# Kernel tuning notes

Measured on AMD Instinct MI355X. Metric: run time of the kernel, lower is better.

## Reference

```python
import jax, jax.numpy as jnp
import numpy as np

B, V_IN, V_OUT, F_IN, F_OUT, N_CP = 100000, 128, 128, 512, 512, 16
DIM_H = max(V_IN, V_OUT)  # hidden_vectors=None -> max(dim_vectors_in, dim_vectors_out)
EPS = 1e-8


def setup_inputs() -> dict:
    key = jax.random.key(0)
    ks = jax.random.split(key, 9)
    u = lambda k, shape, scale: jax.random.uniform(k, shape, jnp.float32, -scale, scale)
    wh_k = 1.0 / np.sqrt(V_IN).astype(np.float32)
    wu_k = 1.0 / np.sqrt(DIM_H + N_CP).astype(np.float32)
    f_in = DIM_H + N_CP + F_IN  # 656
    kf = 1.0 / np.sqrt(f_in).astype(np.float32)
    kg = 1.0 / np.sqrt(F_OUT).astype(np.float32)
    return {
        "feats": jax.random.normal(ks[0], (B, F_IN), jnp.float32),
        "vectors": jax.random.normal(ks[1], (B, V_IN, 3), jnp.float32),
        "Wh": u(ks[2], (V_IN, DIM_H), wh_k),
        "Wcp": u(ks[3], (V_IN, 2 * N_CP), wh_k),
        "Wu": u(ks[4], (DIM_H + N_CP, V_OUT), wu_k),
        "Wf": u(ks[5], (f_in, F_OUT), kf),      # torch Linear weight, stored (in,out)
        "bf": u(ks[6], (F_OUT,), kf),
        "Wg": u(ks[7], (F_OUT, V_OUT), kg),
        "bg": u(ks[8], (V_OUT,), kg),
    }


def reference(feats, vectors, Wh, Wcp, Wu, Wf, bf, Wg, bg):
    # vectors: [b, v_in, 3]; mix vector channels (matmul acts per xyz component c)
    Vh = jnp.einsum('bvc,vh->bhc', vectors, Wh)            # [b, dim_h, 3]
    # cross-product features
    Vcp = jnp.einsum('bvc,vp->bpc', vectors, Wcp)          # [b, 2*n_cp, 3]
    cp = jnp.cross(Vcp[:, :N_CP], Vcp[:, N_CP:])           # [b, n_cp, 3]
    Vh = jnp.concatenate([Vh, cp], axis=1)                 # [b, dim_h+n_cp, 3]
    Vu = jnp.einsum('bkc,ko->boc', Vh, Wu)                 # [b, v_out, 3]
    # clamped L2 norm over xyz
    sh = jnp.sqrt(jnp.maximum(jnp.sum(Vh * Vh, axis=-1), EPS))  # [b, dim_h+n_cp]
    s = jnp.concatenate([feats, sh], axis=1)               # [b, dim_h+n_cp+f_in]
    feats_out = jax.nn.silu(s @ Wf + bf)                   # [b, f_out]
    gating = feats_out @ Wg + bg                           # [b, v_out]
    vectors_out = jax.nn.sigmoid(gating)[..., None] * Vu   # [b, v_out, 3]
    return feats_out, vectors_out
```

## Files before the change

### kernel.cpp

```cpp
#include <hip/hip_runtime.h>

#define BATCH 100000
#define M3 300000
#define VECBASE 51200000
#define KP 704

typedef float fl4  __attribute__((ext_vector_type(4)));
typedef float f32x4 __attribute__((ext_vector_type(4)));
typedef short s16x4 __attribute__((ext_vector_type(4)));
typedef short s16x8 __attribute__((ext_vector_type(8)));

__device__ __forceinline__ short f2bf(float f) {
  unsigned int u = __float_as_uint(f);
  u += 0x7fffu + ((u >> 16) & 1u);
  return (short)(u >> 16);
}
__device__ __forceinline__ float bf2f(short s) {
  return __uint_as_float(((unsigned int)(unsigned short)s) << 16);
}
__device__ __forceinline__ s16x8 pack8(fl4 a, fl4 b) {
  s16x8 o;
  o[0] = f2bf(a[0]); o[1] = f2bf(a[1]); o[2] = f2bf(a[2]); o[3] = f2bf(a[3]);
  o[4] = f2bf(b[0]); o[5] = f2bf(b[1]); o[6] = f2bf(b[2]); o[7] = f2bf(b[3]);
  return o;
}
__device__ __forceinline__ void glds16(const void* g, void* l) {
  __builtin_amdgcn_global_load_lds((const __attribute__((address_space(1))) void*)g,
                                   (__attribute__((address_space(3))) void*)l, 16, 0, 0);
}
#define WAITBAR(N) asm volatile("s_waitcnt vmcnt(" #N ")\ns_barrier" ::: "memory")

__global__ __launch_bounds__(256) void prep_w(
    const float* __restrict__ feats, const float* __restrict__ Wh,
    const float* __restrict__ Wcp, const float* __restrict__ Wu,
    const float* __restrict__ Wf, const float* __restrict__ Wg,
    short* __restrict__ Ab, short* __restrict__ WB1, short* __restrict__ WuTp,
    short* __restrict__ WfT, short* __restrict__ WgT) {
  const int tid = blockIdx.x * 256 + threadIdx.x;
  const int stride = gridDim.x * 256;
  for (int i = tid; i < 6400000; i += stride) {
    int b = i >> 6, kk = (i & 63) * 8;
    fl4 v0 = *reinterpret_cast<const fl4*>(&feats[(size_t)b * 512 + kk]);
    fl4 v1 = *reinterpret_cast<const fl4*>(&feats[(size_t)b * 512 + kk + 4]);
    *(s16x8*)&Ab[(size_t)b * KP + kk] = pack8(v0, v1);
  }
  for (int gid = tid; gid < 466944; gid += stride) {
    if (gid < 20480) {
      int n = gid >> 7, k = gid & 127;
      WB1[gid] = f2bf(n < 128 ? Wh[k * 128 + n] : Wcp[k * 32 + (n - 128)]);
    } else if (gid < 40960) {
      int i = gid - 20480;
      int o = i / 160, k = i - o * 160;
      WuTp[i] = k < 144 ? f2bf(Wu[k * 128 + o]) : (short)0;
    } else if (gid < 401408) {
      int i = gid - 40960;
      int n = i / KP, k = i - n * KP;
      WfT[i] = k < 656 ? f2bf(Wf[k * 512 + n]) : (short)0;
    } else {
      int i = gid - 401408;
      int n = i >> 9, k = i & 511;
      WgT[i] = f2bf(Wg[k * 128 + n]);
    }
  }
}

__global__ __launch_bounds__(256) void geo_fused(
    const float* __restrict__ vecs, const short* __restrict__ WB1,
    const short* __restrict__ WuTp, short* __restrict__ Ab,
    short* __restrict__ Vub) {
  __shared__ __align__(16) short U[96 * 168];
  const int t = threadIdx.x;
  const int b0 = blockIdx.x * 32;
  const int row0 = blockIdx.x * 96;

#pragma unroll
  for (int it = 0; it < 4; ++it) {
    int fi = (it * 256 + t) * 12;
    int bl = fi / 384;
    int rem = fi - bl * 384;
    int v0 = rem / 3;
    const float* p = &vecs[(size_t)(b0 + bl) * 384 + rem];
    fl4 x = *(const fl4*)p, y = *(const fl4*)(p + 4), z = *(const fl4*)(p + 8);
    float vc[3][4] = {{x[0], x[3], y[2], z[1]},
                      {x[1], y[0], y[3], z[2]},
                      {x[2], y[1], z[0], z[3]}};
#pragma unroll
    for (int c = 0; c < 3; ++c) {
      int row = bl * 3 + c;
      s16x4 q;
#pragma unroll
      for (int e = 0; e < 4; ++e) q[e] = f2bf(vc[c][e]);
      int off = (row << 8) + (v0 << 1);
      *(s16x4*)((char*)U + (off ^ ((row & 7) << 4))) = q;
    }
  }
  __syncthreads();

  const int lane = t & 63, wv = t >> 6;
  const int wr = wv >> 1, wc = wv & 1;
  const int lr = lane & 15, lk = lane >> 4;

  {
    f32x4 acc[3][5];
#pragma unroll
    for (int i = 0; i < 3; ++i)
#pragma unroll
      for (int j = 0; j < 5; ++j) acc[i][j] = (f32x4){0.f, 0.f, 0.f, 0.f};
#pragma unroll
    for (int kk = 0; kk < 4; ++kk) {
      s16x8 af[3], bq[5];
#pragma unroll
      for (int mi = 0; mi < 3; ++mi) {
        int row = wr * 48 + mi * 16 + lr;
        int off = (row << 8) + (kk << 6) + (lk << 4);
        af[mi] = *(const s16x8*)((const char*)U + (off ^ ((row & 7) << 4)));
      }
#pragma unroll
      for (int ni = 0; ni < 5; ++ni)
        bq[ni] = *reinterpret_cast<const s16x8*>(
            &WB1[(wc * 80 + ni * 16 + lr) * 128 + (kk << 5) + (lk << 3)]);
      __builtin_amdgcn_s_setprio(1);
#pragma unroll
      for (int mi = 0; mi < 3; ++mi)
#pragma unroll
        for (int ni = 0; ni < 5; ++ni)
          acc[mi][ni] = __builtin_amdgcn_mfma_f32_16x16x32_bf16(af[mi], bq[ni], acc[mi][ni], 0, 0, 0);
      __builtin_amdgcn_s_setprio(0);
    }
    __syncthreads();
#pragma unroll
    for (int mi = 0; mi < 3; ++mi)
#pragma unroll
      for (int ni = 0; ni < 5; ++ni) {
        int col = wc * 80 + ni * 16 + lr;
#pragma unroll
        for (int r = 0; r < 4; ++r) {
          int row = wr * 48 + mi * 16 + lk * 4 + r;
          U[row * 168 + col] = f2bf(acc[mi][ni][r]);
        }
      }
  }
  __syncthreads();

  {
    int bl = t >> 3, pj = t & 7;
    int gb = b0 + bl;
    float shcp[2];
#pragma unroll
    for (int q = 0; q < 2; ++q) {
      int p = pj * 2 + q;
      float ax = bf2f(U[(bl * 3 + 0) * 168 + 128 + p]);
      float ay = bf2f(U[(bl * 3 + 1) * 168 + 128 + p]);
      float az = bf2f(U[(bl * 3 + 2) * 168 + 128 + p]);
      float bx = bf2f(U[(bl * 3 + 0) * 168 + 144 + p]);
      float by = bf2f(U[(bl * 3 + 1) * 168 + 144 + p]);
      float bz = bf2f(U[(bl * 3 + 2) * 168 + 144 + p]);
      float cx = ay * bz - az * by;
      float cy = az * bx - ax * bz;
      float cz = ax * by - ay * bx;
      U[(bl * 3 + 0) * 168 + 128 + p] = f2bf(cx);
      U[(bl * 3 + 1) * 168 + 128 + p] = f2bf(cy);
      U[(bl * 3 + 2) * 168 + 128 + p] = f2bf(cz);
      U[(bl * 3 + 0) * 168 + 144 + p] = 0;
      U[(bl * 3 + 1) * 168 + 144 + p] = 0;
      U[(bl * 3 + 2) * 168 + 144 + p] = 0;
      shcp[q] = sqrtf(fmaxf(cx * cx + cy * cy + cz * cz, 1e-8f));
    }
    Ab[(size_t)gb * KP + 640 + pj * 2]     = f2bf(shcp[0]);
    Ab[(size_t)gb * KP + 640 + pj * 2 + 1] = f2bf(shcp[1]);
#pragma unroll
    for (int z = 0; z < 6; ++z)
      Ab[(size_t)gb * KP + 656 + pj * 6 + z] = 0;
  }
  {
    int bl = t >> 3, kq = t & 7;
    int gb = b0 + bl;
#pragma unroll
    for (int j = 0; j < 2; ++j) {
      int k = kq * 16 + j * 8;
      s16x8 r0 = *(const s16x8*)&U[(bl * 3 + 0) * 168 + k];
      s16x8 r1 = *(const s16x8*)&U[(bl * 3 + 1) * 168 + k];
      s16x8 r2 = *(const s16x8*)&U[(bl * 3 + 2) * 168 + k];
      s16x8 o;
#pragma unroll
      for (int e = 0; e < 8; ++e) {
        float x = bf2f(r0[e]), y = bf2f(r1[e]), z = bf2f(r2[e]);
        o[e] = f2bf(sqrtf(fmaxf(x * x + y * y + z * z, 1e-8f)));
      }
      *(s16x8*)&Ab[(size_t)gb * KP + 512 + k] = o;
    }
  }
  __syncthreads();

  {
    f32x4 acc2[3][4];
#pragma unroll
    for (int i = 0; i < 3; ++i)
#pragma unroll
      for (int j = 0; j < 4; ++j) acc2[i][j] = (f32x4){0.f, 0.f, 0.f, 0.f};
#pragma unroll
    for (int kk = 0; kk < 5; ++kk) {
      s16x8 af[3], bq[4];
#pragma unroll
      for (int mi = 0; mi < 3; ++mi) {
        int row = wr * 48 + mi * 16 + lr;
        af[mi] = *(const s16x8*)&U[row * 168 + (kk << 5) + (lk << 3)];
      }
#pragma unroll
      for (int ni = 0; ni < 4; ++ni)
        bq[ni] = *reinterpret_cast<const s16x8*>(
            &WuTp[(wc * 64 + ni * 16 + lr) * 160 + (kk << 5) + (lk << 3)]);
      __builtin_amdgcn_s_setprio(1);
#pragma unroll
      for (int mi = 0; mi < 3; ++mi)
#pragma unroll
        for (int ni = 0; ni < 4; ++ni)
          acc2[mi][ni] = __builtin_amdgcn_mfma_f32_16x16x32_bf16(af[mi], bq[ni], acc2[mi][ni], 0, 0, 0);
      __builtin_amdgcn_s_setprio(0);
    }
#pragma unroll
    for (int mi = 0; mi < 3; ++mi)
#pragma unroll
      for (int ni = 0; ni < 4; ++ni) {
        int col = wc * 64 + ni * 16 + lr;
#pragma unroll
        for (int r = 0; r < 4; ++r) {
          int row = row0 + wr * 48 + mi * 16 + lk * 4 + r;
          Vub[(size_t)row * 128 + col] = f2bf(acc2[mi][ni][r]);
        }
      }
  }
}

__global__ __launch_bounds__(512, 4) void gemm_feats(
    const short* __restrict__ Ab, const short* __restrict__ WfT,
    const float* __restrict__ bfv, float* __restrict__ out,
    short* __restrict__ fob) {
  const int bid = blockIdx.x;
  const int xcd = bid & 7, bi = bid >> 3;
  const int swz = (xcd < 4 ? xcd * 196 : 784 + (xcd - 4) * 195) + bi;
  const int mt = swz >> 1, nt = swz & 1;
  const int row0 = mt << 7, n0 = nt << 8;
  const int t = threadIdx.x;
  const int lane = t & 63, wv = t >> 6;
  const int wr = wv >> 2, wc = wv & 3;
  const int lr = lane & 15, lk = lane >> 4;

  __shared__ __align__(16) short S[3 * 128 * 32 + 3 * 256 * 32];

  const int arow = t >> 2, ach = t & 3;
  const short* srcA = &Ab[(size_t)min(row0 + arow, BATCH - 1) * KP +
                          ((ach ^ ((arow >> 1) & 3))) * 8];
  const int adof = t * 8;
  const short* srcB[2]; int bdof[2];
#pragma unroll
  for (int j = 0; j < 2; ++j) {
    int cid = j * 512 + t;
    int brow = cid >> 2, bch = cid & 3;
    srcB[j] = &WfT[(size_t)(n0 + brow) * KP + ((bch ^ ((brow >> 1) & 3))) * 8];
    bdof[j] = cid * 8;
  }

  f32x4 acc[4][4];
#pragma unroll
  for (int i = 0; i < 4; ++i)
#pragma unroll
    for (int j = 0; j < 4; ++j) acc[i][j] = (f32x4){0.f, 0.f, 0.f, 0.f};

  auto STAGE = [&](int buf, int ks) {
    const int k0 = ks << 5;
    glds16(srcA + k0, &S[buf * 4096 + adof]);
    glds16(srcB[0] + k0, &S[12288 + buf * 8192 + bdof[0]]);
    glds16(srcB[1] + k0, &S[12288 + buf * 8192 + bdof[1]]);
  };
  auto COMPUTE = [&](int buf) {
    const int ab = buf * 4096, bb = 12288 + buf * 8192;
    s16x8 af[4], bq[4];
#pragma unroll
    for (int mi = 0; mi < 4; ++mi) {
      int rw = wr * 64 + mi * 16 + lr;
      af[mi] = *(const s16x8*)&S[ab + rw * 32 + (lk ^ ((rw >> 1) & 3)) * 8];
    }
#pragma unroll
    for (int ni = 0; ni < 4; ++ni) {
      int rn = wc * 64 + ni * 16 + lr;
      bq[ni] = *(const s16x8*)&S[bb + rn * 32 + (lk ^ ((rn >> 1) & 3)) * 8];
    }
    __builtin_amdgcn_s_setprio(1);
#pragma unroll
    for (int mi = 0; mi < 4; ++mi)
#pragma unroll
      for (int ni = 0; ni < 4; ++ni)
        acc[mi][ni] = __builtin_amdgcn_mfma_f32_16x16x32_bf16(af[mi], bq[ni], acc[mi][ni], 0, 0, 0);
    __builtin_amdgcn_s_setprio(0);
  };

  STAGE(0, 0);
  STAGE(1, 1);
  for (int ks = 0; ks < 22; ++ks) {
    if (ks < 21) WAITBAR(3);
    else         WAITBAR(0);
    COMPUTE(ks % 3);
    if (ks + 2 < 22) STAGE((ks + 2) % 3, ks + 2);
  }

  float* Ls = (float*)S;
#pragma unroll
  for (int g = 0; g < 4; ++g) {
    __syncthreads();
    if (wr == (g >> 1)) {
      int miB = (g & 1) * 2;
#pragma unroll
      for (int m2 = 0; m2 < 2; ++m2) {
#pragma unroll
        for (int ni = 0; ni < 4; ++ni) {
          int colL = wc * 64 + ni * 16 + lr;
          float bb = bfv[n0 + colL];
#pragma unroll
          for (int rr = 0; rr < 4; ++rr) {
            int rowL = m2 * 16 + lk * 4 + rr;
            float x = acc[miB + m2][ni][rr] + bb;
            Ls[rowL * 256 + colL] = x / (1.f + __expf(-x));
          }
        }
      }
    }
    __syncthreads();
    {
      int rowL = t >> 4, seg = t & 15;
      int grow = row0 + g * 32 + rowL;
      if (grow < BATCH) {
        const float* p = &Ls[rowL * 256 + seg * 16];
        fl4 a = *(const fl4*)p, b = *(const fl4*)(p + 4);
        fl4 c = *(const fl4*)(p + 8), d = *(const fl4*)(p + 12);
        float* po = &out[(size_t)grow * 512 + n0 + seg * 16];
        *(fl4*)po = a; *(fl4*)(po + 4) = b; *(fl4*)(po + 8) = c; *(fl4*)(po + 12) = d;
        short* pf = &fob[(size_t)grow * 512 + n0 + seg * 16];
        *(s16x8*)pf = pack8(a, b);
        *(s16x8*)(pf + 8) = pack8(c, d);
      }
    }
  }
}

__global__ __launch_bounds__(512, 4) void gemm_gate(
    const short* __restrict__ fob, const short* __restrict__ WgT,
    const float* __restrict__ bg, const short* __restrict__ Vub,
    float* __restrict__ out) {
  const int bid = blockIdx.x;
  const int xcd = bid & 7, bi = bid >> 3;
  const int swz = (xcd < 7 ? xcd * 49 : 343 + (xcd - 7) * 48) + bi;
  const int row0 = swz << 8;
  const int t = threadIdx.x;
  const int lane = t & 63, wv = t >> 6;
  const int wr = wv >> 1, wc = wv & 1;
  const int lr = lane & 15, lk = lane >> 4;

  __shared__ __align__(16) short S[(256 + 128) * 64];
  short* As = S;
  short* Bs = S + 256 * 64;

  const short* srcA[4]; int adof[4];
#pragma unroll
  for (int j = 0; j < 4; ++j) {
    int cid = j * 512 + t;
    int row = cid >> 3, ch = cid & 7;
    srcA[j] = &fob[(size_t)min(row0 + row, BATCH - 1) * 512 + (ch ^ (row & 7)) * 8];
    adof[j] = cid * 8;
  }
  const short* srcB[2]; int bdof[2];
#pragma unroll
  for (int j = 0; j < 2; ++j) {
    int cid = j * 512 + t;
    int row = cid >> 3, ch = cid & 7;
    srcB[j] = &WgT[(size_t)row * 512 + (ch ^ (row & 7)) * 8];
    bdof[j] = cid * 8;
  }

  f32x4 acc[4][4];
#pragma unroll
  for (int i = 0; i < 4; ++i)
#pragma unroll
    for (int j = 0; j < 4; ++j) acc[i][j] = (f32x4){0.f, 0.f, 0.f, 0.f};

  for (int ks = 0; ks < 8; ++ks) {
    const int k0 = ks << 6;
    __syncthreads();
#pragma unroll
    for (int j = 0; j < 4; ++j) glds16(srcA[j] + k0, &As[adof[j]]);
    glds16(srcB[0] + k0, &Bs[bdof[0]]);
    glds16(srcB[1] + k0, &Bs[bdof[1]]);
    __syncthreads();
#pragma unroll
    for (int kk = 0; kk < 2; ++kk) {
      s16x8 af[4], bq[4];
#pragma unroll
      for (int mi = 0; mi < 4; ++mi) {
        int rw = wr * 64 + mi * 16 + lr;
        af[mi] = *(const s16x8*)&As[rw * 64 + (((kk << 2) + lk) ^ (rw & 7)) * 8];
      }
#pragma unroll
      for (int ni = 0; ni < 4; ++ni) {
        int rn = wc * 64 + ni * 16 + lr;
        bq[ni] = *(const s16x8*)&Bs[rn * 64 + (((kk << 2) + lk) ^ (rn & 7)) * 8];
      }
      __builtin_amdgcn_s_setprio(1);
#pragma unroll
      for (int mi = 0; mi < 4; ++mi)
#pragma unroll
        for (int ni = 0; ni < 4; ++ni)
          acc[mi][ni] = __builtin_amdgcn_mfma_f32_16x16x32_bf16(af[mi], bq[ni], acc[mi][ni], 0, 0, 0);
      __builtin_amdgcn_s_setprio(0);
    }
  }

#pragma unroll
  for (int ni = 0; ni < 4; ++ni) {
    int col = wc * 64 + ni * 16 + lr;
    float bb = bg[col];
#pragma unroll
    for (int mi = 0; mi < 4; ++mi) {
      int rbase = row0 + wr * 64 + mi * 16 + lk * 4;
#pragma unroll
      for (int rr = 0; rr < 4; ++rr) {
        int gr = rbase + rr;
        if (gr < BATCH) {
          float x = acc[mi][ni][rr] + bb;
          float gate = 1.f / (1.f + __expf(-x));
          size_t vb = (size_t)(3 * gr) * 128 + col;
          float* po = &out[VECBASE + ((size_t)gr * 128 + col) * 3];
          po[0] = gate * bf2f(Vub[vb]);
          po[1] = gate * bf2f(Vub[vb + 128]);
          po[2] = gate * bf2f(Vub[vb + 256]);
        }
      }
    }
  }
}

extern "C" void kernel_launch(void* const* d_in, const int* in_sizes, int n_in,
                              void* d_out, int out_size, void* d_ws, size_t ws_size,
                              hipStream_t stream) {
  const float* feats = (const float*)d_in[0];
  const float* vecs  = (const float*)d_in[1];
  const float* Wh    = (const float*)d_in[2];
  const float* Wcp   = (const float*)d_in[3];
  const float* Wu    = (const float*)d_in[4];
  const float* Wf    = (const float*)d_in[5];
  const float* bfv   = (const float*)d_in[6];
  const float* Wg    = (const float*)d_in[7];
  const float* bg    = (const float*)d_in[8];
  float* out = (float*)d_out;

  char* ws = (char*)d_ws;
  short* Ab   = (short*)ws;
  short* Vub  = (short*)(ws + 140800000);
  short* fob  = (short*)(ws + 217600000);
  short* WfT  = (short*)(ws + 320000000);
  short* WgT  = (short*)(ws + 320720896);
  short* WB1  = (short*)(ws + 320851968);
  short* WuTp = (short*)(ws + 320892928);

  hipLaunchKernelGGL(prep_w,     dim3(2048), dim3(256), 0, stream,
                     feats, Wh, Wcp, Wu, Wf, Wg, Ab, WB1, WuTp, WfT, WgT);
  hipLaunchKernelGGL(geo_fused,  dim3(3125), dim3(256), 0, stream,
                     vecs, WB1, WuTp, Ab, Vub);
  hipLaunchKernelGGL(gemm_feats, dim3(1564), dim3(512), 0, stream,
                     Ab, WfT, bfv, out, fob);
  hipLaunchKernelGGL(gemm_gate,  dim3(391),  dim3(512), 0, stream,
                     fob, WgT, bg, Vub, out);
}
```

Measured before the change: 451.9 us.

## Fuse feats bf16 conversion into feature GEMM A-load, drop staging buffer

```diff
diff --git a/kernel.cpp b/kernel.cpp
--- a/kernel.cpp
+++ b/kernel.cpp
@@ -28,45 +28,34 @@
   __builtin_amdgcn_global_load_lds((const __attribute__((address_space(1))) void*)g,
                                    (__attribute__((address_space(3))) void*)l, 16, 0, 0);
 }
-#define WAITBAR(N) asm volatile("s_waitcnt vmcnt(" #N ")\ns_barrier" ::: "memory")
 
 __global__ __launch_bounds__(256) void prep_w(
-    const float* __restrict__ feats, const float* __restrict__ Wh,
-    const float* __restrict__ Wcp, const float* __restrict__ Wu,
-    const float* __restrict__ Wf, const float* __restrict__ Wg,
-    short* __restrict__ Ab, short* __restrict__ WB1, short* __restrict__ WuTp,
-    short* __restrict__ WfT, short* __restrict__ WgT) {
-  const int tid = blockIdx.x * 256 + threadIdx.x;
-  const int stride = gridDim.x * 256;
-  for (int i = tid; i < 6400000; i += stride) {
-    int b = i >> 6, kk = (i & 63) * 8;
-    fl4 v0 = *reinterpret_cast<const fl4*>(&feats[(size_t)b * 512 + kk]);
-    fl4 v1 = *reinterpret_cast<const fl4*>(&feats[(size_t)b * 512 + kk + 4]);
-    *(s16x8*)&Ab[(size_t)b * KP + kk] = pack8(v0, v1);
-  }
-  for (int gid = tid; gid < 466944; gid += stride) {
-    if (gid < 20480) {
-      int n = gid >> 7, k = gid & 127;
-      WB1[gid] = f2bf(n < 128 ? Wh[k * 128 + n] : Wcp[k * 32 + (n - 128)]);
-    } else if (gid < 40960) {
-      int i = gid - 20480;
-      int o = i / 160, k = i - o * 160;
-      WuTp[i] = k < 144 ? f2bf(Wu[k * 128 + o]) : (short)0;
-    } else if (gid < 401408) {
-      int i = gid - 40960;
-      int n = i / KP, k = i - n * KP;
-      WfT[i] = k < 656 ? f2bf(Wf[k * 512 + n]) : (short)0;
-    } else {
-      int i = gid - 401408;
-      int n = i >> 9, k = i & 511;
-      WgT[i] = f2bf(Wg[k * 128 + n]);
-    }
+    const float* __restrict__ Wh, const float* __restrict__ Wcp,
+    const float* __restrict__ Wu, const float* __restrict__ Wf,
+    const float* __restrict__ Wg, short* __restrict__ WB1,
+    short* __restrict__ WuTp, short* __restrict__ WfT, short* __restrict__ WgT) {
+  int gid = blockIdx.x * 256 + threadIdx.x;
+  if (gid < 20480) {
+    int n = gid >> 7, k = gid & 127;
+    WB1[gid] = f2bf(n < 128 ? Wh[k * 128 + n] : Wcp[k * 32 + (n - 128)]);
+  } else if (gid < 40960) {
+    int i = gid - 20480;
+    int o = i / 160, k = i - o * 160;
+    WuTp[i] = k < 144 ? f2bf(Wu[k * 128 + o]) : (short)0;
+  } else if (gid < 401408) {
+    int i = gid - 40960;
+    int n = i / KP, k = i - n * KP;
+    WfT[i] = k < 656 ? f2bf(Wf[k * 512 + n]) : (short)0;
+  } else if (gid < 466944) {
+    int i = gid - 401408;
+    int n = i >> 9, k = i & 511;
+    WgT[i] = f2bf(Wg[k * 128 + n]);
   }
 }
 
 __global__ __launch_bounds__(256) void geo_fused(
     const float* __restrict__ vecs, const short* __restrict__ WB1,
-    const short* __restrict__ WuTp, short* __restrict__ Ab,
+    const short* __restrict__ WuTp, short* __restrict__ shs,
     short* __restrict__ Vub) {
   __shared__ __align__(16) short U[96 * 168];
   const int t = threadIdx.x;
@@ -166,11 +155,11 @@
       U[(bl * 3 + 2) * 168 + 144 + p] = 0;
       shcp[q] = sqrtf(fmaxf(cx * cx + cy * cy + cz * cz, 1e-8f));
     }
-    Ab[(size_t)gb * KP + 640 + pj * 2]     = f2bf(shcp[0]);
-    Ab[(size_t)gb * KP + 640 + pj * 2 + 1] = f2bf(shcp[1]);
+    shs[(size_t)gb * 192 + 128 + pj * 2]     = f2bf(shcp[0]);
+    shs[(size_t)gb * 192 + 128 + pj * 2 + 1] = f2bf(shcp[1]);
 #pragma unroll
     for (int z = 0; z < 6; ++z)
-      Ab[(size_t)gb * KP + 656 + pj * 6 + z] = 0;
+      shs[(size_t)gb * 192 + 144 + pj * 6 + z] = 0;
   }
   {
     int bl = t >> 3, kq = t & 7;
@@ -187,7 +176,7 @@
         float x = bf2f(r0[e]), y = bf2f(r1[e]), z = bf2f(r2[e]);
         o[e] = f2bf(sqrtf(fmaxf(x * x + y * y + z * z, 1e-8f)));
       }
-      *(s16x8*)&Ab[(size_t)gb * KP + 512 + k] = o;
+      *(s16x8*)&shs[(size_t)gb * 192 + k] = o;
     }
   }
   __syncthreads();
@@ -233,9 +222,9 @@
 }
 
 __global__ __launch_bounds__(512, 4) void gemm_feats(
-    const short* __restrict__ Ab, const short* __restrict__ WfT,
-    const float* __restrict__ bfv, float* __restrict__ out,
-    short* __restrict__ fob) {
+    const float* __restrict__ feats, const short* __restrict__ shs,
+    const short* __restrict__ WfT, const float* __restrict__ bfv,
+    float* __restrict__ out, short* __restrict__ fob) {
   const int bid = blockIdx.x;
   const int xcd = bid & 7, bi = bid >> 3;
   const int swz = (xcd < 4 ? xcd * 196 : 784 + (xcd - 4) * 195) + bi;
@@ -246,19 +235,28 @@
   const int wr = wv >> 2, wc = wv & 3;
   const int lr = lane & 15, lk = lane >> 4;
 
-  __shared__ __align__(16) short S[3 * 128 * 32 + 3 * 256 * 32];
-
-  const int arow = t >> 2, ach = t & 3;
-  const short* srcA = &Ab[(size_t)min(row0 + arow, BATCH - 1) * KP +
-                          ((ach ^ ((arow >> 1) & 3))) * 8];
-  const int adof = t * 8;
-  const short* srcB[2]; int bdof[2];
+  __shared__ __align__(16) short S[(128 + 256) * 64];
+
+  const int arow = t >> 2, aq = t & 3;
+  const size_t arowc = (size_t)min(row0 + arow, BATCH - 1);
+  const float* aFp = &feats[arowc * 512 + aq * 16];
+  const int aw0 = arow * 64 + (((aq * 2) ^ (arow & 7)) << 3);
+  const int aw1 = arow * 64 + (((aq * 2 + 1) ^ (arow & 7)) << 3);
+  const short* srcAs[2]; int adofs[2];
 #pragma unroll
   for (int j = 0; j < 2; ++j) {
     int cid = j * 512 + t;
-    int brow = cid >> 2, bch = cid & 3;
-    srcB[j] = &WfT[(size_t)(n0 + brow) * KP + ((bch ^ ((brow >> 1) & 3))) * 8];
-    bdof[j] = cid * 8;
+    int row = cid >> 3, ch = cid & 7;
+    srcAs[j] = &shs[(size_t)min(row0 + row, BATCH - 1) * 192 + ((ch ^ (row & 7)) * 8)];
+    adofs[j] = cid * 8;
+  }
+  const short* srcB[4]; int bdof[4];
+#pragma unroll
+  for (int j = 0; j < 4; ++j) {
+    int cid = j * 512 + t;
+    int row = cid >> 3, ch = cid & 7;
+    srcB[j] = &WfT[(size_t)(n0 + row) * KP + (ch ^ (row & 7)) * 8];
+    bdof[j] = 8192 + cid * 8;
   }
 
   f32x4 acc[4][4];
@@ -267,41 +265,50 @@
 #pragma unroll
     for (int j = 0; j < 4; ++j) acc[i][j] = (f32x4){0.f, 0.f, 0.f, 0.f};
 
-  auto STAGE = [&](int buf, int ks) {
-    const int k0 = ks << 5;
-    glds16(srcA + k0, &S[buf * 4096 + adof]);
-    glds16(srcB[0] + k0, &S[12288 + buf * 8192 + bdof[0]]);
-    glds16(srcB[1] + k0, &S[12288 + buf * 8192 + bdof[1]]);
+  fl4 frA[4];
+  auto loadA = [&](int ks) {
+    const float* p = aFp + (ks << 6);
+    frA[0] = *(const fl4*)p;       frA[1] = *(const fl4*)(p + 4);
+    frA[2] = *(const fl4*)(p + 8); frA[3] = *(const fl4*)(p + 12);
   };
-  auto COMPUTE = [&](int buf) {
-    const int ab = buf * 4096, bb = 12288 + buf * 8192;
-    s16x8 af[4], bq[4];
-#pragma unroll
-    for (int mi = 0; mi < 4; ++mi) {
-      int rw = wr * 64 + mi * 16 + lr;
-      af[mi] = *(const s16x8*)&S[ab + rw * 32 + (lk ^ ((rw >> 1) & 3)) * 8];
-    }
-#pragma unroll
-    for (int ni = 0; ni < 4; ++ni) {
-      int rn = wc * 64 + ni * 16 + lr;
-      bq[ni] = *(const s16x8*)&S[bb + rn * 32 + (lk ^ ((rn >> 1) & 3)) * 8];
-    }
-    __builtin_amdgcn_s_setprio(1);
-#pragma unroll
-    for (int mi = 0; mi < 4; ++mi)
-#pragma unroll
-      for (int ni = 0; ni < 4; ++ni)
-        acc[mi][ni] = __builtin_amdgcn_mfma_f32_16x16x32_bf16(af[mi], bq[ni], acc[mi][ni], 0, 0, 0);
-    __builtin_amdgcn_s_setprio(0);
-  };
-
-  STAGE(0, 0);
-  STAGE(1, 1);
-  for (int ks = 0; ks < 22; ++ks) {
-    if (ks < 21) WAITBAR(3);
-    else         WAITBAR(0);
-    COMPUTE(ks % 3);
-    if (ks + 2 < 22) STAGE((ks + 2) % 3, ks + 2);
+
+  loadA(0);
+  for (int ks = 0; ks < 11; ++ks) {
+    __syncthreads();
+    if (ks < 8) {
+      *(s16x8*)&S[aw0] = pack8(frA[0], frA[1]);
+      *(s16x8*)&S[aw1] = pack8(frA[2], frA[3]);
+    } else {
+      const int ko = (ks - 8) << 6;
+      glds16(srcAs[0] + ko, &S[adofs[0]]);
+      glds16(srcAs[1] + ko, &S[adofs[1]]);
+    }
+    const int k0 = ks << 6;
+#pragma unroll
+    for (int j = 0; j < 4; ++j) glds16(srcB[j] + k0, &S[bdof[j]]);
+    __syncthreads();
+    if (ks + 1 < 8) loadA(ks + 1);
+#pragma unroll
+    for (int kk = 0; kk < 2; ++kk) {
+      s16x8 af[4], bq[4];
+#pragma unroll
+      for (int mi = 0; mi < 4; ++mi) {
+        int rw = wr * 64 + mi * 16 + lr;
+        af[mi] = *(const s16x8*)&S[rw * 64 + (((kk << 2) + lk) ^ (rw & 7)) * 8];
+      }
+#pragma unroll
+      for (int ni = 0; ni < 4; ++ni) {
+        int rn = wc * 64 + ni * 16 + lr;
+        bq[ni] = *(const s16x8*)&S[8192 + rn * 64 + (((kk << 2) + lk) ^ (rn & 7)) * 8];
+      }
+      __builtin_amdgcn_s_setprio(1);
+#pragma unroll
+      for (int mi = 0; mi < 4; ++mi)
+#pragma unroll
+        for (int ni = 0; ni < 4; ++ni)
+          acc[mi][ni] = __builtin_amdgcn_mfma_f32_16x16x32_bf16(af[mi], bq[ni], acc[mi][ni], 0, 0, 0);
+      __builtin_amdgcn_s_setprio(0);
+    }
   }
 
   float* Ls = (float*)S;
@@ -453,20 +460,20 @@
   float* out = (float*)d_out;
 
   char* ws = (char*)d_ws;
-  short* Ab   = (short*)ws;
-  short* Vub  = (short*)(ws + 140800000);
-  short* fob  = (short*)(ws + 217600000);
-  short* WfT  = (short*)(ws + 320000000);
-  short* WgT  = (short*)(ws + 320720896);
-  short* WB1  = (short*)(ws + 320851968);
-  short* WuTp = (short*)(ws + 320892928);
-
-  hipLaunchKernelGGL(prep_w,     dim3(2048), dim3(256), 0, stream,
-                     feats, Wh, Wcp, Wu, Wf, Wg, Ab, WB1, WuTp, WfT, WgT);
+  short* shs  = (short*)ws;
+  short* Vub  = (short*)(ws + 38400000);
+  short* fob  = (short*)(ws + 115200000);
+  short* WfT  = (short*)(ws + 217600000);
+  short* WgT  = (short*)(ws + 218320896);
+  short* WB1  = (short*)(ws + 218451968);
+  short* WuTp = (short*)(ws + 218492928);
+
+  hipLaunchKernelGGL(prep_w,     dim3(1824), dim3(256), 0, stream,
+                     Wh, Wcp, Wu, Wf, Wg, WB1, WuTp, WfT, WgT);
   hipLaunchKernelGGL(geo_fused,  dim3(3125), dim3(256), 0, stream,
-                     vecs, WB1, WuTp, Ab, Vub);
+                     vecs, WB1, WuTp, shs, Vub);
   hipLaunchKernelGGL(gemm_feats, dim3(1564), dim3(512), 0, stream,
-                     Ab, WfT, bfv, out, fob);
+                     feats, shs, WfT, bfv, out, fob);
   hipLaunchKernelGGL(gemm_gate,  dim3(391),  dim3(512), 0, stream,
                      fob, WgT, bg, Vub, out);
 }
```

After: 435.1 us. 3.7% less time.
